# Optimization experiments

Hardware: AMD Instinct MI355X
Metric: run time of the kernel (lower is better)

Reference implementation:

```python
import jax, jax.numpy as jnp
import numpy as np

EMB_DIM = 1024
N_EXPERTS = 8
TOP_K = 2
MOE_HIDDEN = 1024
NORM_TOPK = True


def setup_inputs() -> dict:
    key = jax.random.key(0)
    ks = jax.random.split(key, 7)
    s = 0.02
    return {
        "x": jax.random.normal(ks[0], (2, 2048, EMB_DIM), dtype=jnp.float32),
        "router_w": jax.random.normal(ks[1], (N_EXPERTS, EMB_DIM), dtype=jnp.float32) * s,
        "router_b": jnp.zeros((N_EXPERTS,), dtype=jnp.float32),
        "gate_up_w": jax.random.normal(ks[2], (N_EXPERTS, 2 * MOE_HIDDEN, EMB_DIM), dtype=jnp.float32) * s,
        "gate_up_b": jnp.zeros((N_EXPERTS, 2 * MOE_HIDDEN), dtype=jnp.float32),
        "down_w": jax.random.normal(ks[3], (N_EXPERTS, EMB_DIM, MOE_HIDDEN), dtype=jnp.float32) * s,
        "down_b": jnp.zeros((N_EXPERTS, EMB_DIM), dtype=jnp.float32),
    }


def _swiglu(h):
    # SwiGLUFFN: even columns gate, odd columns up
    gate = h[:, ::2]
    up = h[:, 1::2]
    return jnp.clip(gate, -7.0, 7.0) * jax.nn.sigmoid(1.702 * gate) * (jnp.clip(up, -7.0, 7.0) + 1.0)


def reference(x, router_w, router_b, gate_up_w, gate_up_b, down_w, down_b):
    B, S, D = x.shape
    h = x.reshape(B * S, D)  # [T, D]
    # Router: linear -> top-k -> (softmax over k)
    scores = h @ router_w.T + router_b  # [T, E]
    vals, idx = jax.lax.top_k(scores, TOP_K)  # [T, K]
    if NORM_TOPK:
        vals = jax.nn.softmax(vals, axis=-1)
    # Combine weights per (token, expert); zero for unselected experts, so
    # masked-dense compute below is mathematically identical to gather/scatter.
    cw = jnp.sum(jax.nn.one_hot(idx, N_EXPERTS, dtype=vals.dtype) * vals[..., None], axis=1)  # [T, E]
    out = jnp.zeros_like(h)
    for e in range(N_EXPERTS):  # fixed small expert count
        g = h @ gate_up_w[e].T + gate_up_b[e]  # [T, 2H]
        a = _swiglu(g)  # [T, H]
        oe = a @ down_w[e].T + down_b[e]  # [T, D]
        out = out + oe * cw[:, e:e + 1]
    return out.reshape(B, S, D)
```

## Files before the change

### kernel.cpp

```cpp
#include <hip/hip_runtime.h>
#include <hip/hip_bf16.h>

#define EMB 1024
#define NEXP 8
#define NH 1024
#define N_GU 2048
#define TOPK 2

#define BM 128
#define BN 128
#define BK 64
#define KTILES 16
#define MAXTILES 72

typedef __attribute__((ext_vector_type(4))) float f32x4;
typedef __attribute__((ext_vector_type(8))) short s16x8;
typedef __attribute__((ext_vector_type(4))) short s16x4;

typedef __attribute__((address_space(3))) unsigned int lds_u32;
typedef __attribute__((address_space(1))) const unsigned int glb_u32;

__device__ __forceinline__ void gl_lds16(const void* g, void* l) {
  __builtin_amdgcn_global_load_lds((glb_u32*)g, (lds_u32*)l, 16, 0, 0);
}

__device__ __forceinline__ unsigned short f2bf(float f) {
  union { float f; unsigned int u; } a; a.f = f;
  unsigned int u = a.u;
  unsigned int r = (u + 0x7FFFu + ((u >> 16) & 1u)) >> 16;
  return (unsigned short)r;
}

__device__ __forceinline__ float b2f(unsigned short h) {
  union { unsigned int u; float f; } a;
  a.u = ((unsigned int)h) << 16;
  return a.f;
}

__device__ __forceinline__ int xcd_swz(int bid, int nwg) {
  int q = nwg >> 3, r = nwg & 7;
  int xcd = bid & 7, pos = bid >> 3;
  int base = (xcd < r) ? xcd * (q + 1) : r * (q + 1) + (xcd - r) * q;
  return base + pos;
}

__global__ void convert_router(const float* __restrict__ x, unsigned short* __restrict__ xb, int n4x,
                               const float* __restrict__ guw, unsigned short* __restrict__ guwb, int n4g,
                               const float* __restrict__ dw, unsigned short* __restrict__ dwb, int n4d,
                               const float* __restrict__ rw, const float* __restrict__ rb, int T,
                               int* __restrict__ tokE, float* __restrict__ tokW) {
  int nr = T / 4;
  if ((int)blockIdx.x < nr) {
    int gwid = blockIdx.x * 4 + (threadIdx.x >> 6);
    int lane = threadIdx.x & 63;
    if (gwid >= T) return;
    const float* h = x + (size_t)gwid * EMB;
    float hreg[16];
    #pragma unroll
    for (int i = 0; i < 16; ++i) hreg[i] = h[lane + 64 * i];
    float sc[NEXP];
    #pragma unroll
    for (int e = 0; e < NEXP; ++e) {
      const float* w = rw + e * EMB;
      float s = 0.f;
      #pragma unroll
      for (int i = 0; i < 16; ++i) s += hreg[i] * w[lane + 64 * i];
      #pragma unroll
      for (int off = 32; off > 0; off >>= 1) s += __shfl_xor(s, off);
      sc[e] = s + rb[e];
    }
    if (lane == 0) {
      int e0 = 0; float v0 = sc[0];
      #pragma unroll
      for (int e = 1; e < NEXP; ++e) if (sc[e] > v0) { v0 = sc[e]; e0 = e; }
      int e1 = -1; float v1 = -3.0e38f;
      #pragma unroll
      for (int e = 0; e < NEXP; ++e) { if (e == e0) continue; if (sc[e] > v1) { v1 = sc[e]; e1 = e; } }
      float ex = __expf(v1 - v0);
      float w0 = 1.f / (1.f + ex);
      float w1 = ex / (1.f + ex);
      tokE[gwid * 2] = e0; tokE[gwid * 2 + 1] = e1;
      tokW[gwid * 2] = w0; tokW[gwid * 2 + 1] = w1;
    }
  } else {
    int tot = n4x + n4g + n4d;
    int base = (blockIdx.x - nr) * blockDim.x + threadIdx.x;
    int stride = (gridDim.x - nr) * blockDim.x;
    for (int i = base; i < tot; i += stride) {
      const float* src; unsigned short* dst; int k;
      if (i < n4x) { src = x; dst = xb; k = i; }
      else if (i < n4x + n4g) { src = guw; dst = guwb; k = i - n4x; }
      else { src = dw; dst = dwb; k = i - n4x - n4g; }
      float4 v = ((const float4*)src)[k];
      s16x4 o;
      o[0] = (short)f2bf(v.x);
      o[1] = (short)f2bf(v.y);
      o[2] = (short)f2bf(v.z);
      o[3] = (short)f2bf(v.w);
      ((s16x4*)dst)[k] = o;
    }
  }
}

__global__ void meta_scatter(const int* __restrict__ tokE, int A,
                             int* __restrict__ tilemeta,
                             int* __restrict__ rows, int* __restrict__ apos) {
  __shared__ int hist[NEXP];
  __shared__ int offs[NEXP];
  __shared__ int fill[NEXP];
  int t = threadIdx.x;
  if (t < NEXP) { hist[t] = 0; fill[t] = 0; }
  __syncthreads();
  for (int i = t; i < A; i += blockDim.x) atomicAdd(&hist[tokE[i]], 1);
  __syncthreads();
  if (t == 0) {
    int off = 0, nt = 0;
    for (int e = 0; e < NEXP; ++e) {
      offs[e] = off;
      int c = hist[e];
      int ntile = (c + BM - 1) / BM;
      for (int k = 0; k < ntile; ++k) {
        tilemeta[1 + nt * 3 + 0] = e;
        tilemeta[1 + nt * 3 + 1] = off + k * BM;
        tilemeta[1 + nt * 3 + 2] = off + c;
        nt++;
      }
      off += c;
    }
    tilemeta[0] = nt;
  }
  __syncthreads();
  for (int i = t; i < A; i += blockDim.x) {
    int e = tokE[i];
    int p = offs[e] + atomicAdd(&fill[e], 1);
    rows[p] = i >> 1;
    apos[i] = p;
  }
}

__global__ __launch_bounds__(256, 4) void gemm_gate_up(
    const unsigned short* __restrict__ xb,
    const unsigned short* __restrict__ gub,
    const float* __restrict__ gu_bias,
    const int* __restrict__ rows,
    const int* __restrict__ tilemeta,
    unsigned short* __restrict__ hact) {
  __shared__ __align__(16) short As[BM * BK];
  __shared__ __align__(16) short Bs[BN * BK];
  int wg = xcd_swz(blockIdx.x, gridDim.x);
  int tileid = wg >> 4;
  int n0 = (wg & 15) * BN;
  int nt = tilemeta[0];
  if (tileid >= nt) return;
  int e    = tilemeta[1 + tileid * 3 + 0];
  int m0   = tilemeta[1 + tileid * 3 + 1];
  int mEnd = tilemeta[1 + tileid * 3 + 2];

  int t = threadIdx.x;
  int lane = t & 63;
  int wid = t >> 6;
  int wr = wid >> 1, wc = wid & 1;

  int srow = lane >> 3;
  int scol = (((lane & 7) ^ (srow & 7)) * 8);
  const unsigned short* ga[4];
  const unsigned short* gb[4];
  int dstoff[4];
  #pragma unroll
  for (int q = 0; q < 4; ++q) {
    int rt = wid * 32 + q * 8 + srow;
    int ai = m0 + rt; if (ai >= mEnd) ai = mEnd - 1;
    ga[q] = xb + (size_t)rows[ai] * EMB + scol;
    gb[q] = gub + ((size_t)e * N_GU + n0 + rt) * EMB + scol;
    dstoff[q] = (wid * 32 + q * 8) * BK;
  }

  int fr = lane & 15;
  int q8 = (lane >> 4) * 8;
  int rsw = (fr & 7) << 3;

  f32x4 acc[4][4];
  #pragma unroll
  for (int i = 0; i < 4; ++i)
    #pragma unroll
    for (int j = 0; j < 4; ++j) acc[i][j] = (f32x4){0.f, 0.f, 0.f, 0.f};

  for (int tk = 0; tk < KTILES; ++tk) {
    int k0 = tk * BK;
    __syncthreads();
    #pragma unroll
    for (int q = 0; q < 4; ++q) {
      gl_lds16(ga[q] + k0, &As[dstoff[q]]);
      gl_lds16(gb[q] + k0, &Bs[dstoff[q]]);
    }
    __syncthreads();
    #pragma unroll
    for (int kk = 0; kk < BK; kk += 32) {
      s16x8 a[4], b[4];
      #pragma unroll
      for (int i = 0; i < 4; ++i)
        a[i] = *(const s16x8*)(&As[(wr * 64 + i * 16 + fr) * BK + ((kk + q8) ^ rsw)]);
      #pragma unroll
      for (int j = 0; j < 4; ++j)
        b[j] = *(const s16x8*)(&Bs[(wc * 64 + j * 16 + fr) * BK + ((kk + q8) ^ rsw)]);
      #pragma unroll
      for (int i = 0; i < 4; ++i)
        #pragma unroll
        for (int j = 0; j < 4; ++j)
          acc[i][j] = __builtin_amdgcn_mfma_f32_16x16x32_bf16(a[i], b[j], acc[i][j], 0, 0, 0);
    }
  }

  const float* bias_e = gu_bias + (size_t)e * N_GU;
  int rbase = m0 + wr * 64 + ((lane >> 4) * 4);
  #pragma unroll
  for (int i = 0; i < 4; ++i) {
    #pragma unroll
    for (int j = 0; j < 4; ++j) {
      int n = n0 + wc * 64 + j * 16 + fr;
      float v[4], o[4];
      #pragma unroll
      for (int r = 0; r < 4; ++r) v[r] = acc[i][j][r] + bias_e[n];
      #pragma unroll
      for (int r = 0; r < 4; ++r) o[r] = __shfl_xor(v[r], 1);
      if ((lane & 1) == 0) {
        int outc = n >> 1;
        #pragma unroll
        for (int r = 0; r < 4; ++r) {
          int pos = rbase + i * 16 + r;
          if (pos < mEnd) {
            float g = v[r], u = o[r];
            float gc = fminf(fmaxf(g, -7.f), 7.f);
            float uc = fminf(fmaxf(u, -7.f), 7.f);
            float sig = 1.f / (1.f + __expf(-1.702f * g));
            float act = gc * sig * (uc + 1.f);
            hact[(size_t)pos * NH + outc] = f2bf(act);
          }
        }
      }
    }
  }
}

__global__ __launch_bounds__(256, 4) void gemm_down(
    const unsigned short* __restrict__ hact,
    const unsigned short* __restrict__ dwb,
    const int* __restrict__ tilemeta,
    unsigned short* __restrict__ y) {
  __shared__ __align__(16) short As[BM * BK];
  __shared__ __align__(16) short Bs[BN * BK];
  int wg = xcd_swz(blockIdx.x, gridDim.x);
  int tileid = wg >> 3;
  int n0 = (wg & 7) * BN;
  int nt = tilemeta[0];
  if (tileid >= nt) return;
  int e    = tilemeta[1 + tileid * 3 + 0];
  int m0   = tilemeta[1 + tileid * 3 + 1];
  int mEnd = tilemeta[1 + tileid * 3 + 2];

  int t = threadIdx.x;
  int lane = t & 63;
  int wid = t >> 6;
  int wr = wid >> 1, wc = wid & 1;

  int srow = lane >> 3;
  int scol = (((lane & 7) ^ (srow & 7)) * 8);
  const unsigned short* ga[4];
  const unsigned short* gb[4];
  int dstoff[4];
  #pragma unroll
  for (int q = 0; q < 4; ++q) {
    int rt = wid * 32 + q * 8 + srow;
    int ai = m0 + rt; if (ai >= mEnd) ai = mEnd - 1;
    ga[q] = hact + (size_t)ai * NH + scol;
    gb[q] = dwb + ((size_t)e * EMB + n0 + rt) * NH + scol;
    dstoff[q] = (wid * 32 + q * 8) * BK;
  }

  int fr = lane & 15;
  int q8 = (lane >> 4) * 8;
  int rsw = (fr & 7) << 3;

  f32x4 acc[4][4];
  #pragma unroll
  for (int i = 0; i < 4; ++i)
    #pragma unroll
    for (int j = 0; j < 4; ++j) acc[i][j] = (f32x4){0.f, 0.f, 0.f, 0.f};

  for (int tk = 0; tk < KTILES; ++tk) {
    int k0 = tk * BK;
    __syncthreads();
    #pragma unroll
    for (int q = 0; q < 4; ++q) {
      gl_lds16(ga[q] + k0, &As[dstoff[q]]);
      gl_lds16(gb[q] + k0, &Bs[dstoff[q]]);
    }
    __syncthreads();
    #pragma unroll
    for (int kk = 0; kk < BK; kk += 32) {
      s16x8 a[4], b[4];
      #pragma unroll
      for (int i = 0; i < 4; ++i)
        a[i] = *(const s16x8*)(&As[(wr * 64 + i * 16 + fr) * BK + ((kk + q8) ^ rsw)]);
      #pragma unroll
      for (int j = 0; j < 4; ++j)
        b[j] = *(const s16x8*)(&Bs[(wc * 64 + j * 16 + fr) * BK + ((kk + q8) ^ rsw)]);
      #pragma unroll
      for (int i = 0; i < 4; ++i)
        #pragma unroll
        for (int j = 0; j < 4; ++j)
          acc[i][j] = __builtin_amdgcn_mfma_f32_16x16x32_bf16(a[i], b[j], acc[i][j], 0, 0, 0);
    }
  }

  int rbase = m0 + wr * 64 + ((lane >> 4) * 4);
  #pragma unroll
  for (int i = 0; i < 4; ++i) {
    #pragma unroll
    for (int j = 0; j < 4; ++j) {
      int n = n0 + wc * 64 + j * 16 + fr;
      #pragma unroll
      for (int r = 0; r < 4; ++r) {
        int pos = rbase + i * 16 + r;
        if (pos < mEnd) y[(size_t)pos * EMB + n] = f2bf(acc[i][j][r]);
      }
    }
  }
}

__global__ void combine_out(const unsigned short* __restrict__ y, const float* __restrict__ down_b,
                            const int* __restrict__ tokE, const float* __restrict__ tokW,
                            const int* __restrict__ apos, float* __restrict__ out, int T) {
  int i = blockIdx.x * blockDim.x + threadIdx.x;
  int tot = T * (EMB / 4);
  if (i >= tot) return;
  int tok = i >> 8;
  int c = i & 255;
  int e0 = tokE[tok * 2], e1 = tokE[tok * 2 + 1];
  float w0 = tokW[tok * 2], w1 = tokW[tok * 2 + 1];
  int p0 = apos[tok * 2], p1 = apos[tok * 2 + 1];
  s16x4 v0 = ((const s16x4*)(y + (size_t)p0 * EMB))[c];
  s16x4 v1 = ((const s16x4*)(y + (size_t)p1 * EMB))[c];
  float4 b0 = ((const float4*)(down_b + (size_t)e0 * EMB))[c];
  float4 b1 = ((const float4*)(down_b + (size_t)e1 * EMB))[c];
  float4 o;
  o.x = w0 * (b2f((unsigned short)v0[0]) + b0.x) + w1 * (b2f((unsigned short)v1[0]) + b1.x);
  o.y = w0 * (b2f((unsigned short)v0[1]) + b0.y) + w1 * (b2f((unsigned short)v1[1]) + b1.y);
  o.z = w0 * (b2f((unsigned short)v0[2]) + b0.z) + w1 * (b2f((unsigned short)v1[2]) + b1.z);
  o.w = w0 * (b2f((unsigned short)v0[3]) + b0.w) + w1 * (b2f((unsigned short)v1[3]) + b1.w);
  ((float4*)out)[i] = o;
}

extern "C" void kernel_launch(void* const* d_in, const int* in_sizes, int n_in,
                              void* d_out, int out_size, void* d_ws, size_t ws_size,
                              hipStream_t stream) {
  const float* x   = (const float*)d_in[0];
  const float* rw  = (const float*)d_in[1];
  const float* rb  = (const float*)d_in[2];
  const float* guw = (const float*)d_in[3];
  const float* gub = (const float*)d_in[4];
  const float* dw  = (const float*)d_in[5];
  const float* db  = (const float*)d_in[6];
  float* out = (float*)d_out;

  int T = in_sizes[0] / EMB;
  int A = T * TOPK;

  char* ws = (char*)d_ws;
  size_t off = 0;
  auto alloc = [&](size_t bytes) -> void* {
    void* p = ws + off;
    off = (off + bytes + 255) & ~((size_t)255);
    return p;
  };
  unsigned short* xb   = (unsigned short*)alloc((size_t)T * EMB * 2);
  unsigned short* guwb = (unsigned short*)alloc((size_t)NEXP * N_GU * EMB * 2);
  unsigned short* dwb  = (unsigned short*)alloc((size_t)NEXP * EMB * NH * 2);
  unsigned short* hact = (unsigned short*)alloc((size_t)A * NH * 2);
  unsigned short* y    = (unsigned short*)alloc((size_t)A * EMB * 2);
  int*   tokE    = (int*)alloc((size_t)A * 4);
  float* tokW    = (float*)alloc((size_t)A * 4);
  int*   apos    = (int*)alloc((size_t)A * 4);
  int*   rowsArr = (int*)alloc((size_t)A * 4);
  int*   tilemeta= (int*)alloc((1 + MAXTILES * 3) * 4);

  int n4x = T * EMB / 4;
  int n4g = NEXP * N_GU * EMB / 4;
  int n4d = NEXP * EMB * NH / 4;
  convert_router<<<T / 4 + 2048, 256, 0, stream>>>(x, xb, n4x, guw, guwb, n4g, dw, dwb, n4d,
                                                   rw, rb, T, tokE, tokW);

  meta_scatter<<<1, 1024, 0, stream>>>(tokE, A, tilemeta, rowsArr, apos);

  gemm_gate_up<<<MAXTILES * (N_GU / BN), 256, 0, stream>>>(xb, guwb, gub, rowsArr, tilemeta, hact);
  gemm_down<<<MAXTILES * (EMB / BN), 256, 0, stream>>>(hact, dwb, tilemeta, y);

  combine_out<<<(T * EMB / 4 + 255) / 256, 256, 0, stream>>>(y, db, tokE, tokW, apos, out, T);
}
```

Measured before the change: 140.0 us.

## Double M tile to 256 rows with 8 waves per block in expert GEMMs

Raises the row tile from 128 to 256 and the block size from 256 to 512 threads (8 waves, a 4x2 wave grid) in both the gate-up and down GEMMs. The global-to-LDS load mapping is rewritten so A tiles take four loads per thread and B tiles two. Each weight tile is now reused across twice as many token rows, which cuts weight traffic and the number of tiles (MAXTILES drops to 40). In exchange LDS per block rises, more rows are padded waste for small expert groups, and fewer blocks may fit per CU.

```diff
diff --git a/kernel.cpp b/kernel.cpp
--- a/kernel.cpp
+++ b/kernel.cpp
@@ -7,11 +7,11 @@
 #define N_GU 2048
 #define TOPK 2
 
-#define BM 128
+#define BM 256
 #define BN 128
 #define BK 64
 #define KTILES 16
-#define MAXTILES 72
+#define MAXTILES 40
 
 typedef __attribute__((ext_vector_type(4))) float f32x4;
 typedef __attribute__((ext_vector_type(8))) short s16x8;
@@ -138,7 +138,7 @@
   }
 }
 
-__global__ __launch_bounds__(256, 4) void gemm_gate_up(
+__global__ __launch_bounds__(512, 4) void gemm_gate_up(
     const unsigned short* __restrict__ xb,
     const unsigned short* __restrict__ gub,
     const float* __restrict__ gu_bias,
@@ -159,20 +159,26 @@
   int t = threadIdx.x;
   int lane = t & 63;
   int wid = t >> 6;
-  int wr = wid >> 1, wc = wid & 1;
+  int wr = wid >> 1;
+  int wc = wid & 1;
 
   int srow = lane >> 3;
   int scol = (((lane & 7) ^ (srow & 7)) * 8);
   const unsigned short* ga[4];
-  const unsigned short* gb[4];
-  int dstoff[4];
+  const unsigned short* gb[2];
+  int dstA[4], dstB[2];
   #pragma unroll
   for (int q = 0; q < 4; ++q) {
-    int rt = wid * 32 + q * 8 + srow;
+    int rt = q * 64 + wid * 8 + srow;
     int ai = m0 + rt; if (ai >= mEnd) ai = mEnd - 1;
     ga[q] = xb + (size_t)rows[ai] * EMB + scol;
+    dstA[q] = (q * 64 + wid * 8) * BK;
+  }
+  #pragma unroll
+  for (int q = 0; q < 2; ++q) {
+    int rt = q * 64 + wid * 8 + srow;
     gb[q] = gub + ((size_t)e * N_GU + n0 + rt) * EMB + scol;
-    dstoff[q] = (wid * 32 + q * 8) * BK;
+    dstB[q] = (q * 64 + wid * 8) * BK;
   }
 
   int fr = lane & 15;
@@ -189,10 +195,9 @@
     int k0 = tk * BK;
     __syncthreads();
     #pragma unroll
-    for (int q = 0; q < 4; ++q) {
-      gl_lds16(ga[q] + k0, &As[dstoff[q]]);
-      gl_lds16(gb[q] + k0, &Bs[dstoff[q]]);
-    }
+    for (int q = 0; q < 4; ++q) gl_lds16(ga[q] + k0, &As[dstA[q]]);
+    #pragma unroll
+    for (int q = 0; q < 2; ++q) gl_lds16(gb[q] + k0, &Bs[dstB[q]]);
     __syncthreads();
     #pragma unroll
     for (int kk = 0; kk < BK; kk += 32) {
@@ -242,7 +247,7 @@
   }
 }
 
-__global__ __launch_bounds__(256, 4) void gemm_down(
+__global__ __launch_bounds__(512, 4) void gemm_down(
     const unsigned short* __restrict__ hact,
     const unsigned short* __restrict__ dwb,
     const int* __restrict__ tilemeta,
@@ -261,20 +266,26 @@
   int t = threadIdx.x;
   int lane = t & 63;
   int wid = t >> 6;
-  int wr = wid >> 1, wc = wid & 1;
+  int wr = wid >> 1;
+  int wc = wid & 1;
 
   int srow = lane >> 3;
   int scol = (((lane & 7) ^ (srow & 7)) * 8);
   const unsigned short* ga[4];
-  const unsigned short* gb[4];
-  int dstoff[4];
+  const unsigned short* gb[2];
+  int dstA[4], dstB[2];
   #pragma unroll
   for (int q = 0; q < 4; ++q) {
-    int rt = wid * 32 + q * 8 + srow;
+    int rt = q * 64 + wid * 8 + srow;
     int ai = m0 + rt; if (ai >= mEnd) ai = mEnd - 1;
     ga[q] = hact + (size_t)ai * NH + scol;
+    dstA[q] = (q * 64 + wid * 8) * BK;
+  }
+  #pragma unroll
+  for (int q = 0; q < 2; ++q) {
+    int rt = q * 64 + wid * 8 + srow;
     gb[q] = dwb + ((size_t)e * EMB + n0 + rt) * NH + scol;
-    dstoff[q] = (wid * 32 + q * 8) * BK;
+    dstB[q] = (q * 64 + wid * 8) * BK;
   }
 
   int fr = lane & 15;
@@ -291,10 +302,9 @@
     int k0 = tk * BK;
     __syncthreads();
     #pragma unroll
-    for (int q = 0; q < 4; ++q) {
-      gl_lds16(ga[q] + k0, &As[dstoff[q]]);
-      gl_lds16(gb[q] + k0, &Bs[dstoff[q]]);
-    }
+    for (int q = 0; q < 4; ++q) gl_lds16(ga[q] + k0, &As[dstA[q]]);
+    #pragma unroll
+    for (int q = 0; q < 2; ++q) gl_lds16(gb[q] + k0, &Bs[dstB[q]]);
     __syncthreads();
     #pragma unroll
     for (int kk = 0; kk < BK; kk += 32) {
@@ -392,8 +402,8 @@
 
   meta_scatter<<<1, 1024, 0, stream>>>(tokE, A, tilemeta, rowsArr, apos);
 
-  gemm_gate_up<<<MAXTILES * (N_GU / BN), 256, 0, stream>>>(xb, guwb, gub, rowsArr, tilemeta, hact);
-  gemm_down<<<MAXTILES * (EMB / BN), 256, 0, stream>>>(hact, dwb, tilemeta, y);
+  gemm_gate_up<<<MAXTILES * (N_GU / BN), 512, 0, stream>>>(xb, guwb, gub, rowsArr, tilemeta, hact);
+  gemm_down<<<MAXTILES * (EMB / BN), 512, 0, stream>>>(hact, dwb, tilemeta, y);
 
   combine_out<<<(T * EMB / 4 + 255) / 256, 256, 0, stream>>>(y, db, tokE, tokW, apos, out, T);
 }
```

Measured after the change: 148.8 us. +6.3%, slower.

## Use 256x256 double-buffered pipelined tiles for gate-up GEMM with separate tile metadata

Applied to the files above, without the earlier changes.

Rewrites the gate_up grouped GEMM to use 256x256 tiles with 512 threads and double-buffered LDS. Global-to-LDS loads for the next K-tile are interleaved with MFMA phases under fine-grained vmcnt waits, barriers and s_setprio. meta_scatter now emits two tile lists, 256-row tiles for gate_up and 128-row tiles for down. This aims to raise data reuse per tile and hide load latency, at the cost of more padded rows per expert, fewer workgroups and higher register pressure.

```diff
diff --git a/kernel.cpp b/kernel.cpp
--- a/kernel.cpp
+++ b/kernel.cpp
@@ -7,11 +7,16 @@
 #define N_GU 2048
 #define TOPK 2
 
+#define BMg 256
+#define BNg 256
+#define BKg 64
+#define MAXT256 40
+
 #define BM 128
 #define BN 128
 #define BK 64
 #define KTILES 16
-#define MAXTILES 72
+#define MAXT128 72
 
 typedef __attribute__((ext_vector_type(4))) float f32x4;
 typedef __attribute__((ext_vector_type(8))) short s16x8;
@@ -103,7 +108,7 @@
 }
 
 __global__ void meta_scatter(const int* __restrict__ tokE, int A,
-                             int* __restrict__ tilemeta,
+                             int* __restrict__ tm256, int* __restrict__ tm128,
                              int* __restrict__ rows, int* __restrict__ apos) {
   __shared__ int hist[NEXP];
   __shared__ int offs[NEXP];
@@ -114,20 +119,28 @@
   for (int i = t; i < A; i += blockDim.x) atomicAdd(&hist[tokE[i]], 1);
   __syncthreads();
   if (t == 0) {
-    int off = 0, nt = 0;
+    int off = 0, nt2 = 0, nt1 = 0;
     for (int e = 0; e < NEXP; ++e) {
       offs[e] = off;
       int c = hist[e];
-      int ntile = (c + BM - 1) / BM;
-      for (int k = 0; k < ntile; ++k) {
-        tilemeta[1 + nt * 3 + 0] = e;
-        tilemeta[1 + nt * 3 + 1] = off + k * BM;
-        tilemeta[1 + nt * 3 + 2] = off + c;
-        nt++;
+      int n2 = (c + BMg - 1) / BMg;
+      for (int k = 0; k < n2; ++k) {
+        tm256[1 + nt2 * 3 + 0] = e;
+        tm256[1 + nt2 * 3 + 1] = off + k * BMg;
+        tm256[1 + nt2 * 3 + 2] = off + c;
+        nt2++;
+      }
+      int n1 = (c + BM - 1) / BM;
+      for (int k = 0; k < n1; ++k) {
+        tm128[1 + nt1 * 3 + 0] = e;
+        tm128[1 + nt1 * 3 + 1] = off + k * BM;
+        tm128[1 + nt1 * 3 + 2] = off + c;
+        nt1++;
       }
       off += c;
     }
-    tilemeta[0] = nt;
+    tm256[0] = nt2;
+    tm128[0] = nt1;
   }
   __syncthreads();
   for (int i = t; i < A; i += blockDim.x) {
@@ -138,18 +151,53 @@
   }
 }
 
-__global__ __launch_bounds__(256, 4) void gemm_gate_up(
+#define VM4 asm volatile("s_waitcnt vmcnt(4)" ::: "memory")
+#define VM2 asm volatile("s_waitcnt vmcnt(2)" ::: "memory")
+#define NOW
+#define PHASE(buf, mh, nh, LOADA, STAGE, WAIT) do {                                          \
+  if (LOADA) {                                                                               \
+    _Pragma("unroll")                                                                        \
+    for (int mf = 0; mf < 4; ++mf) {                                                         \
+      int rowa = wr * 128 + (mh) * 64 + mf * 16 + fr;                                        \
+      af[mf][0] = *(const s16x8*)(&As[buf][rowa * BKg + ((q8) ^ rsw)]);                      \
+      af[mf][1] = *(const s16x8*)(&As[buf][rowa * BKg + ((32 + q8) ^ rsw)]);                 \
+    }                                                                                        \
+  }                                                                                          \
+  s16x8 bf[2][2];                                                                            \
+  _Pragma("unroll")                                                                          \
+  for (int j = 0; j < 2; ++j) {                                                              \
+    int rowb = wc * 64 + ((nh) * 2 + j) * 16 + fr;                                           \
+    bf[j][0] = *(const s16x8*)(&Bs[buf][rowb * BKg + ((q8) ^ rsw)]);                         \
+    bf[j][1] = *(const s16x8*)(&Bs[buf][rowb * BKg + ((32 + q8) ^ rsw)]);                    \
+  }                                                                                          \
+  STAGE;                                                                                     \
+  __builtin_amdgcn_s_setprio(1);                                                             \
+  _Pragma("unroll")                                                                          \
+  for (int mf = 0; mf < 4; ++mf)                                                             \
+    _Pragma("unroll")                                                                        \
+    for (int j = 0; j < 2; ++j) {                                                            \
+      acc[(mh)*4+mf][(nh)*2+j] = __builtin_amdgcn_mfma_f32_16x16x32_bf16(af[mf][0], bf[j][0], acc[(mh)*4+mf][(nh)*2+j], 0, 0, 0); \
+      acc[(mh)*4+mf][(nh)*2+j] = __builtin_amdgcn_mfma_f32_16x16x32_bf16(af[mf][1], bf[j][1], acc[(mh)*4+mf][(nh)*2+j], 0, 0, 0); \
+    }                                                                                        \
+  __builtin_amdgcn_s_setprio(0);                                                             \
+  WAIT;                                                                                      \
+  asm volatile("" ::: "memory");                                                             \
+  __builtin_amdgcn_s_barrier();                                                              \
+  asm volatile("" ::: "memory");                                                             \
+} while (0)
+
+__global__ __launch_bounds__(512, 2) void gemm_gate_up(
     const unsigned short* __restrict__ xb,
     const unsigned short* __restrict__ gub,
     const float* __restrict__ gu_bias,
     const int* __restrict__ rows,
     const int* __restrict__ tilemeta,
     unsigned short* __restrict__ hact) {
-  __shared__ __align__(16) short As[BM * BK];
-  __shared__ __align__(16) short Bs[BN * BK];
+  __shared__ __align__(16) short As[2][BMg * BKg];
+  __shared__ __align__(16) short Bs[2][BNg * BKg];
   int wg = xcd_swz(blockIdx.x, gridDim.x);
-  int tileid = wg >> 4;
-  int n0 = (wg & 15) * BN;
+  int tileid = wg >> 3;
+  int n0 = (wg & 7) * BNg;
   int nt = tilemeta[0];
   if (tileid >= nt) return;
   int e    = tilemeta[1 + tileid * 3 + 0];
@@ -159,75 +207,75 @@
   int t = threadIdx.x;
   int lane = t & 63;
   int wid = t >> 6;
-  int wr = wid >> 1, wc = wid & 1;
-
-  int srow = lane >> 3;
-  int scol = (((lane & 7) ^ (srow & 7)) * 8);
-  const unsigned short* ga[4];
-  const unsigned short* gb[4];
-  int dstoff[4];
+  int wr = wid >> 2;
+  int wc = wid & 3;
+
+  int srow = t >> 3;
+  int schunk = t & 7;
+  int scol = ((schunk ^ (srow & 7)) * 8);
+  const unsigned short* gaQ[4];
+  const unsigned short* gbQ[4];
+  int dstQ[4];
   #pragma unroll
   for (int q = 0; q < 4; ++q) {
-    int rt = wid * 32 + q * 8 + srow;
-    int ai = m0 + rt; if (ai >= mEnd) ai = mEnd - 1;
-    ga[q] = xb + (size_t)rows[ai] * EMB + scol;
-    gb[q] = gub + ((size_t)e * N_GU + n0 + rt) * EMB + scol;
-    dstoff[q] = (wid * 32 + q * 8) * BK;
+    int ai = m0 + q * 64 + srow; if (ai >= mEnd) ai = mEnd - 1;
+    gaQ[q] = xb + (size_t)rows[ai] * EMB + scol;
+    gbQ[q] = gub + ((size_t)e * N_GU + n0 + q * 64 + srow) * EMB + scol;
+    dstQ[q] = (q * 64 + srow) * BKg + schunk * 8;
   }
 
   int fr = lane & 15;
   int q8 = (lane >> 4) * 8;
   int rsw = (fr & 7) << 3;
 
-  f32x4 acc[4][4];
-  #pragma unroll
-  for (int i = 0; i < 4; ++i)
+  f32x4 acc[8][4];
+  #pragma unroll
+  for (int i = 0; i < 8; ++i)
     #pragma unroll
     for (int j = 0; j < 4; ++j) acc[i][j] = (f32x4){0.f, 0.f, 0.f, 0.f};
-
-  for (int tk = 0; tk < KTILES; ++tk) {
-    int k0 = tk * BK;
-    __syncthreads();
-    #pragma unroll
-    for (int q = 0; q < 4; ++q) {
-      gl_lds16(ga[q] + k0, &As[dstoff[q]]);
-      gl_lds16(gb[q] + k0, &Bs[dstoff[q]]);
-    }
-    __syncthreads();
-    #pragma unroll
-    for (int kk = 0; kk < BK; kk += 32) {
-      s16x8 a[4], b[4];
-      #pragma unroll
-      for (int i = 0; i < 4; ++i)
-        a[i] = *(const s16x8*)(&As[(wr * 64 + i * 16 + fr) * BK + ((kk + q8) ^ rsw)]);
-      #pragma unroll
-      for (int j = 0; j < 4; ++j)
-        b[j] = *(const s16x8*)(&Bs[(wc * 64 + j * 16 + fr) * BK + ((kk + q8) ^ rsw)]);
-      #pragma unroll
-      for (int i = 0; i < 4; ++i)
-        #pragma unroll
-        for (int j = 0; j < 4; ++j)
-          acc[i][j] = __builtin_amdgcn_mfma_f32_16x16x32_bf16(a[i], b[j], acc[i][j], 0, 0, 0);
-    }
+  s16x8 af[4][2];
+
+  #define SA(buf, q, kt) gl_lds16(gaQ[q] + (kt) * BKg, &As[buf][dstQ[q]])
+  #define SB(buf, q, kt) gl_lds16(gbQ[q] + (kt) * BKg, &Bs[buf][dstQ[q]])
+
+  SB(0, 0, 0); SB(0, 1, 0); SB(0, 2, 0); SB(0, 3, 0);
+  SA(0, 0, 0); SA(0, 2, 0); SA(0, 1, 0); SA(0, 3, 0);
+  VM2;
+  asm volatile("" ::: "memory");
+  __builtin_amdgcn_s_barrier();
+  asm volatile("" ::: "memory");
+
+  for (int i = 0; i < KTILES / 2; ++i) {
+    int t1 = 2 * i + 1;
+    int t2 = 2 * i + 2;
+    bool st = (t2 < KTILES);
+    PHASE(0, 0, 0, true,  { SB(1, 0, t1); SB(1, 1, t1); }, NOW);
+    PHASE(0, 0, 1, false, { SB(1, 2, t1); SB(1, 3, t1); }, VM4);
+    PHASE(0, 1, 0, true,  { SA(1, 0, t1); SA(1, 2, t1); }, NOW);
+    PHASE(0, 1, 1, false, { SA(1, 1, t1); SA(1, 3, t1); }, VM2);
+    PHASE(1, 0, 0, true,  { if (st) { SB(0, 0, t2); SB(0, 1, t2); } }, NOW);
+    PHASE(1, 0, 1, false, { if (st) { SB(0, 2, t2); SB(0, 3, t2); } }, VM4);
+    PHASE(1, 1, 0, true,  { if (st) { SA(0, 0, t2); SA(0, 2, t2); } }, NOW);
+    PHASE(1, 1, 1, false, { if (st) { SA(0, 1, t2); SA(0, 3, t2); } }, VM2);
   }
 
   const float* bias_e = gu_bias + (size_t)e * N_GU;
-  int rbase = m0 + wr * 64 + ((lane >> 4) * 4);
-  #pragma unroll
-  for (int i = 0; i < 4; ++i) {
-    #pragma unroll
-    for (int j = 0; j < 4; ++j) {
-      int n = n0 + wc * 64 + j * 16 + fr;
+  #pragma unroll
+  for (int mi = 0; mi < 8; ++mi) {
+    int rbase = m0 + wr * 128 + mi * 16 + ((lane >> 4) * 4);
+    #pragma unroll
+    for (int nf = 0; nf < 4; ++nf) {
+      int n = n0 + wc * 64 + nf * 16 + fr;
       float v[4], o[4];
       #pragma unroll
-      for (int r = 0; r < 4; ++r) v[r] = acc[i][j][r] + bias_e[n];
+      for (int r = 0; r < 4; ++r) v[r] = acc[mi][nf][r] + bias_e[n];
       #pragma unroll
       for (int r = 0; r < 4; ++r) o[r] = __shfl_xor(v[r], 1);
       if ((lane & 1) == 0) {
         int outc = n >> 1;
         #pragma unroll
         for (int r = 0; r < 4; ++r) {
-          int pos = rbase + i * 16 + r;
+          int pos = rbase + r;
           if (pos < mEnd) {
             float g = v[r], u = o[r];
             float gc = fminf(fmaxf(g, -7.f), 7.f);
@@ -382,7 +430,8 @@
   float* tokW    = (float*)alloc((size_t)A * 4);
   int*   apos    = (int*)alloc((size_t)A * 4);
   int*   rowsArr = (int*)alloc((size_t)A * 4);
-  int*   tilemeta= (int*)alloc((1 + MAXTILES * 3) * 4);
+  int*   tm256   = (int*)alloc((1 + MAXT256 * 3) * 4);
+  int*   tm128   = (int*)alloc((1 + MAXT128 * 3) * 4);
 
   int n4x = T * EMB / 4;
   int n4g = NEXP * N_GU * EMB / 4;
@@ -390,10 +439,10 @@
   convert_router<<<T / 4 + 2048, 256, 0, stream>>>(x, xb, n4x, guw, guwb, n4g, dw, dwb, n4d,
                                                    rw, rb, T, tokE, tokW);
 
-  meta_scatter<<<1, 1024, 0, stream>>>(tokE, A, tilemeta, rowsArr, apos);
-
-  gemm_gate_up<<<MAXTILES * (N_GU / BN), 256, 0, stream>>>(xb, guwb, gub, rowsArr, tilemeta, hact);
-  gemm_down<<<MAXTILES * (EMB / BN), 256, 0, stream>>>(hact, dwb, tilemeta, y);
+  meta_scatter<<<1, 1024, 0, stream>>>(tokE, A, tm256, tm128, rowsArr, apos);
+
+  gemm_gate_up<<<MAXT256 * (N_GU / BNg), 512, 0, stream>>>(xb, guwb, gub, rowsArr, tm256, hact);
+  gemm_down<<<MAXT128 * (EMB / BN), 256, 0, stream>>>(hact, dwb, tm128, y);
 
   combine_out<<<(T * EMB / 4 + 255) / 256, 256, 0, stream>>>(y, db, tokE, tokW, apos, out, T);
 }
```

New measurement: 171.0 us. +22.1%, slower.

## Overlap down-weight bf16 conversion with gate-up GEMM via extra blocks

Applied to the files above, without the earlier changes.

Moves conversion of the down-projection weights from the first conversion kernel into extra blocks appended to the gate-up GEMM launch. The up-front conversion kernel becomes shorter, and the down-weight conversion is meant to run alongside the gate-up GEMM on otherwise idle CUs. The conversion blocks have the highest block indices, so they may only be scheduled after the GEMM tiles, and their memory traffic can compete with the GEMM's loads. The XCD swizzle now uses the fixed GEMM grid size.

```diff
diff --git a/kernel.cpp b/kernel.cpp
--- a/kernel.cpp
+++ b/kernel.cpp
@@ -12,6 +12,8 @@
 #define BK 64
 #define KTILES 16
 #define MAXTILES 72
+#define GRID_GU (MAXTILES * 16)
+#define CONV_BLKS 256
 
 typedef __attribute__((ext_vector_type(4))) float f32x4;
 typedef __attribute__((ext_vector_type(8))) short s16x8;
@@ -46,7 +48,6 @@
 
 __global__ void convert_router(const float* __restrict__ x, unsigned short* __restrict__ xb, int n4x,
                                const float* __restrict__ guw, unsigned short* __restrict__ guwb, int n4g,
-                               const float* __restrict__ dw, unsigned short* __restrict__ dwb, int n4d,
                                const float* __restrict__ rw, const float* __restrict__ rb, int T,
                                int* __restrict__ tokE, float* __restrict__ tokW) {
   int nr = T / 4;
@@ -83,14 +84,13 @@
       tokW[gwid * 2] = w0; tokW[gwid * 2 + 1] = w1;
     }
   } else {
-    int tot = n4x + n4g + n4d;
+    int tot = n4x + n4g;
     int base = (blockIdx.x - nr) * blockDim.x + threadIdx.x;
     int stride = (gridDim.x - nr) * blockDim.x;
     for (int i = base; i < tot; i += stride) {
       const float* src; unsigned short* dst; int k;
       if (i < n4x) { src = x; dst = xb; k = i; }
-      else if (i < n4x + n4g) { src = guw; dst = guwb; k = i - n4x; }
-      else { src = dw; dst = dwb; k = i - n4x - n4g; }
+      else { src = guw; dst = guwb; k = i - n4x; }
       float4 v = ((const float4*)src)[k];
       s16x4 o;
       o[0] = (short)f2bf(v.x);
@@ -144,10 +144,25 @@
     const float* __restrict__ gu_bias,
     const int* __restrict__ rows,
     const int* __restrict__ tilemeta,
-    unsigned short* __restrict__ hact) {
+    unsigned short* __restrict__ hact,
+    const float* __restrict__ dw, unsigned short* __restrict__ dwb, int n4d) {
   __shared__ __align__(16) short As[BM * BK];
   __shared__ __align__(16) short Bs[BN * BK];
-  int wg = xcd_swz(blockIdx.x, gridDim.x);
+  if ((int)blockIdx.x >= GRID_GU) {
+    int base = ((int)blockIdx.x - GRID_GU) * blockDim.x + threadIdx.x;
+    int stride = CONV_BLKS * blockDim.x;
+    for (int i = base; i < n4d; i += stride) {
+      float4 v = ((const float4*)dw)[i];
+      s16x4 o;
+      o[0] = (short)f2bf(v.x);
+      o[1] = (short)f2bf(v.y);
+      o[2] = (short)f2bf(v.z);
+      o[3] = (short)f2bf(v.w);
+      ((s16x4*)dwb)[i] = o;
+    }
+    return;
+  }
+  int wg = xcd_swz(blockIdx.x, GRID_GU);
   int tileid = wg >> 4;
   int n0 = (wg & 15) * BN;
   int nt = tilemeta[0];
@@ -387,12 +402,13 @@
   int n4x = T * EMB / 4;
   int n4g = NEXP * N_GU * EMB / 4;
   int n4d = NEXP * EMB * NH / 4;
-  convert_router<<<T / 4 + 2048, 256, 0, stream>>>(x, xb, n4x, guw, guwb, n4g, dw, dwb, n4d,
+  convert_router<<<T / 4 + 2048, 256, 0, stream>>>(x, xb, n4x, guw, guwb, n4g,
                                                    rw, rb, T, tokE, tokW);
 
   meta_scatter<<<1, 1024, 0, stream>>>(tokE, A, tilemeta, rowsArr, apos);
 
-  gemm_gate_up<<<MAXTILES * (N_GU / BN), 256, 0, stream>>>(xb, guwb, gub, rowsArr, tilemeta, hact);
+  gemm_gate_up<<<GRID_GU + CONV_BLKS, 256, 0, stream>>>(xb, guwb, gub, rowsArr, tilemeta, hact,
+                                                        dw, dwb, n4d);
   gemm_down<<<MAXTILES * (EMB / BN), 256, 0, stream>>>(hact, dwb, tilemeta, y);
 
   combine_out<<<(T * EMB / 4 + 255) / 256, 256, 0, stream>>>(y, db, tokE, tokW, apos, out, T);
```

Result: faster. 136.2 us (-2.7%).
